# Kernel optimization log

Measured on AMD Instinct MI355X. Metric: run time of the kernel, lower is better.

## Reference

```python
import jax, jax.numpy as jnp
from jax import lax
import numpy as np

K_RAW, S_RAW, P_RAW = 4, 2, 1
K_CORR, S_CORR, P_CORR, D_CORR = 3, 1, 1, 1
FUSE_K = 3
SOFTMAX_SCALE = 10.0
NEG_BIG = -1e9  # stands in for -inf added to masked patches (softmax -> ~0)


def _patches(img, k, s, p, d=1):
    # (n,c,h,w) -> (n, c*k*k, ho, wo); channel ordering (c, kh, kw) matches torch.nn.functional.unfold
    return lax.conv_general_dilated_patches(img, (k, k), (s, s), [(p, p), (p, p)], rhs_dilation=(d, d))


def _conv_eye(m, kern):
    # 2D conv with the 'eye' fuse kernel, stride 1, same padding
    pad = (FUSE_K - 1) // 2
    return lax.conv_general_dilated(m, kern, (1, 1), [(pad, pad), (pad, pad)],
                                    dimension_numbers=('NCHW', 'OIHW', 'NCHW'))


def _deconv(score, filt, k, s, p):
    # torch conv_transpose2d for one sample: score (L,h,w), filt (L,c,k,k) -> (c, H, W)
    rhs = jnp.flip(filt.transpose(1, 0, 2, 3), (2, 3))  # (c, L, k, k), spatially flipped
    pad = k - 1 - p
    out = lax.conv_general_dilated(score[None], rhs, (1, 1), [(pad, pad), (pad, pad)],
                                   lhs_dilation=(s, s),
                                   dimension_numbers=('NCHW', 'OIHW', 'NCHW'))
    return out[0]


def _forward(x, context, mask):
    n, c, h, w = x.shape
    # --- raw context patches (patch-copy filters), torch unfold order ---
    raw_p = _patches(context, K_RAW, S_RAW, P_RAW)           # (n, c*16, hr, wr)
    hr, wr = raw_p.shape[2], raw_p.shape[3]
    Lr = hr * wr
    raw_filter = raw_p.reshape(n, c * K_RAW * K_RAW, Lr).transpose(0, 2, 1)
    raw_filter = raw_filter.reshape(n, Lr, c, K_RAW, K_RAW)
    xs = x[:, :, ::2, ::2]
    cs = context[:, :, ::2, ::2]
    # --- L2-normalized context patches for correlation ---
    cp = _patches(cs, K_CORR, S_CORR, P_CORR, D_CORR)        # (n, c*9, hu, wu)
    hu, wu = cp.shape[2], cp.shape[3]
    L = hu * wu
    cols = cp.reshape(n, c * K_CORR * K_CORR, L).transpose(0, 2, 1)  # (n, L, c*9)
    norm = jnp.sqrt(jnp.sum(cols * cols, axis=2, keepdims=True))
    cols = cols / jnp.maximum(norm, jnp.asarray(1e-4, cols.dtype))
    # --- patch correlation: grouped conv == einsum over unfolded x ---
    xp = _patches(xs, K_CORR, S_CORR, P_CORR, D_CORR)        # (n, c*9, hm, wm)
    hm, wm = xp.shape[2], xp.shape[3]
    corr = jnp.einsum('nkhw,nlk->nlhw', xp, cols)            # (n, L, hm, wm)
    # --- fuse correlation map with eye kernels (literal translation) ---
    eye = jnp.eye(FUSE_K, dtype=corr.dtype).reshape(1, 1, FUSE_K, FUSE_K)
    m_ = corr.transpose(0, 2, 3, 1).reshape(n, 1, hm * wm, hu * wu)
    m_ = _conv_eye(m_, eye)
    m_ = m_.reshape(n, hu, wu, hm, wm).transpose(0, 2, 1, 4, 3).reshape(n, 1, hu * wu, hm * wm)
    m_ = _conv_eye(m_, eye)
    corr = m_.reshape(n, wu, hu, wm, hm).transpose(0, 4, 3, 2, 1).reshape(n, -1, hu, wu)
    # --- mask: any masked pixel in a patch => patch excluded from softmax ---
    ms = mask[:, :, ::2, ::2]
    mp = _patches(ms, K_CORR, S_CORR, P_CORR, D_CORR)        # (n, 9, hu, wu)
    masked = (jnp.sum(mp, axis=1) > 0).reshape(n, L, 1, 1)
    corr = corr + jnp.where(masked, jnp.asarray(NEG_BIG, corr.dtype), jnp.asarray(0.0, corr.dtype))
    # --- softmax over patch dim ---
    att = jax.nn.softmax(corr * SOFTMAX_SCALE, axis=1)       # (n, L, hu, wu)
    # --- weighted patch copy via per-sample conv_transpose ---
    out = jax.vmap(lambda a, f: _deconv(a, f, K_RAW, S_RAW, P_RAW))(att, raw_filter)  # (n, c, h, w)
    # --- overlap normalization ---
    ones_in = jnp.ones((1, hu, wu), att.dtype)
    ones_f = jnp.ones((1, 1, K_RAW, K_RAW), att.dtype)
    overlap = _deconv(ones_in, ones_f, K_RAW, S_RAW, P_RAW)  # (1, h, w)
    overlap = jnp.where(overlap == 0, jnp.asarray(1.0, att.dtype), overlap)
    out = out / overlap[None]
    att_score = att.reshape(n, hu, wu, hu, wu)
    return out, att_score


def setup_inputs() -> dict:
    key = jax.random.key(0)
    k1, k2 = jax.random.split(key)
    N, C, H, W = 4, 96, 96, 96
    x = jax.random.normal(k1, (N, C, H, W), jnp.float32)
    context = jax.random.normal(k2, (N, C, H, W), jnp.float32)
    # rectangular inpainting hole (1 = masked), as in DeepFill training
    mask = jnp.zeros((N, 1, H, W), jnp.float32).at[:, :, 32:64, 32:64].set(1.0)
    return {"x": x, "context": context, "mask": mask}


def reference(x, context, mask):
    return _forward(x, context, mask)
```

## Files before the change

kernel.cpp:

```cpp
#include <hip/hip_runtime.h>
#include <stdint.h>

#define BN_ 4
#define CC 96
#define HF 96
#define WF 96
#define HS 48
#define WS 48
#define LL 2304
#define J2 1536
#define NEG10 (-1.0e10f)
#define NLS 32

typedef __attribute__((ext_vector_type(8))) _Float16 half8v;
typedef __attribute__((ext_vector_type(4))) float float4v;
typedef float float4u __attribute__((ext_vector_type(4), aligned(4)));

__device__ __forceinline__ int Tswap(int f) { return (f % 48) * 48 + f / 48; }

__device__ __forceinline__ unsigned short f2h(float f) {
    _Float16 h = (_Float16)f;
    return __builtin_bit_cast(unsigned short, h);
}
__device__ __forceinline__ float h2f(unsigned short u) {
    return (float)__builtin_bit_cast(_Float16, u);
}

typedef const __attribute__((address_space(1))) uint32_t* gas_ptr;
typedef __attribute__((address_space(3))) uint32_t* las_ptr;
__device__ __forceinline__ void gload16(const void* g, void* l) {
    __builtin_amdgcn_global_load_lds((gas_ptr)g, (las_ptr)l, 16, 0, 0);
}

__global__ void ssum_kernel(const float* __restrict__ ctx, float* __restrict__ ssum) {
    int idx = blockIdx.x * 256 + threadIdx.x;
    if (idx >= BN_ * HS * WS) return;
    int j = idx % WS, i = (idx / WS) % HS, n = idx / (WS * HS);
    float s = 0.f;
    for (int c = 0; c < CC; ++c) {
        float v = ctx[((size_t)(n * CC + c) * HF + 2 * i) * WF + 2 * j];
        s += v * v;
    }
    ssum[idx] = s;
}

__global__ void invnmask_kernel(const float* __restrict__ ssum, const float* __restrict__ mask,
                                float* __restrict__ invn, float* __restrict__ maskadd) {
    int idx = blockIdx.x * 256 + threadIdx.x;
    if (idx >= BN_ * LL) return;
    int l = idx % LL, n = idx / LL;
    int i0 = l / WS, j0 = l % WS;
    float s = 0.f, ms = 0.f;
    for (int dy = -1; dy <= 1; ++dy)
        for (int dx = -1; dx <= 1; ++dx) {
            int i = i0 + dy, j = j0 + dx;
            if (i >= 0 && i < HS && j >= 0 && j < WS) {
                s += ssum[(n * HS + i) * WS + j];
                ms += mask[(size_t)n * HF * WF + (2 * i) * WF + 2 * j];
            }
        }
    invn[idx] = 1.f / fmaxf(sqrtf(s), 1e-4f);
    maskadd[idx] = (ms > 0.f) ? NEG10 : 0.f;
}

__global__ void slice_split2(const float* __restrict__ ctx, const float* __restrict__ x,
                             unsigned short* __restrict__ cs_hi, unsigned short* __restrict__ cs_lo,
                             unsigned short* __restrict__ xs_hi, unsigned short* __restrict__ xs_lo) {
    int idx = blockIdx.x * 256 + threadIdx.x;
    if (idx >= BN_ * LL * CC) return;
    const float* src = blockIdx.y ? x : ctx;
    unsigned short* hi = blockIdx.y ? xs_hi : cs_hi;
    unsigned short* lo = blockIdx.y ? xs_lo : cs_lo;
    int c = idx % CC;
    int u = (idx / CC) % LL;
    int n = idx / (CC * LL);
    int i = u / WS, j = u % WS;
    float v = src[((size_t)(n * CC + c) * HF + 2 * i) * WF + 2 * j];
    unsigned short h = f2h(v);
    hi[idx] = h;
    lo[idx] = f2h(v - h2f(h));
}

__global__ void rf_split(const float* __restrict__ ctx, unsigned short* __restrict__ hf) {
    int idx = blockIdx.x * 256 + threadIdx.x;
    if (idx >= BN_ * J2 * LL) return;
    int l = idx % LL;
    int j = (idx / LL) % J2;
    int n = idx / (LL * J2);
    int c = j >> 4, ky = (j >> 2) & 3, kx = j & 3;
    int y = 2 * (l / WS) + ky - 1;
    int x = 2 * (l % WS) + kx - 1;
    float v = 0.f;
    if (y >= 0 && y < HF && x >= 0 && x < WF)
        v = ctx[((size_t)(n * CC + c) * HF + y) * WF + x];
    hf[idx] = f2h(v);
}

__global__ __launch_bounds__(256, 4) void gemm_split3(
    const unsigned short* __restrict__ Ah_, const unsigned short* __restrict__ Al_,
    const unsigned short* __restrict__ Bh_, const unsigned short* __restrict__ Bl_,
    float* __restrict__ Cout, int M_, int N_, int K_, int nbx, int nby)
{
    __shared__ unsigned short lds[4][128][32];

    int wg = blockIdx.x;
    int wgid = (wg & 7) * (gridDim.x >> 3) + (wg >> 3);
    int bx = wgid % nbx;
    int t1 = wgid / nbx;
    int by = t1 % nby;
    int bz = t1 / nby;
    const int m0 = by * 128, n0 = bx * 128;
    const int t = threadIdx.x;

    const size_t sA = (size_t)M_ * K_, sB = (size_t)N_ * K_;
    const unsigned short* Ah = Ah_ + (size_t)bz * sA;
    const unsigned short* Al = Al_ + (size_t)bz * sA;
    const unsigned short* Bh = Bh_ + (size_t)bz * sB;
    const unsigned short* Bl = Bl_ + (size_t)bz * sB;

    const int rloc = t >> 2;
    const int sst = t & 3;
    const int kg = sst ^ ((rloc >> 1) & 3);
    const size_t offA0 = (size_t)(m0 + rloc) * K_ + kg * 8;
    const size_t offA1 = (size_t)(m0 + 64 + rloc) * K_ + kg * 8;
    const size_t offB0 = (size_t)(n0 + rloc) * K_ + kg * 8;
    const size_t offB1 = (size_t)(n0 + 64 + rloc) * K_ + kg * 8;
    const unsigned short* gp0 = Ah + offA0;
    const unsigned short* gp1 = Ah + offA1;
    const unsigned short* gp2 = Al + offA0;
    const unsigned short* gp3 = Al + offA1;
    const unsigned short* gp4 = Bh + offB0;
    const unsigned short* gp5 = Bh + offB1;
    const unsigned short* gp6 = Bl + offB0;
    const unsigned short* gp7 = Bl + offB1;
    unsigned short* lp0 = &lds[0][rloc][sst * 8];
    unsigned short* lp1 = &lds[0][64 + rloc][sst * 8];
    unsigned short* lp2 = &lds[1][rloc][sst * 8];
    unsigned short* lp3 = &lds[1][64 + rloc][sst * 8];
    unsigned short* lp4 = &lds[2][rloc][sst * 8];
    unsigned short* lp5 = &lds[2][64 + rloc][sst * 8];
    unsigned short* lp6 = &lds[3][rloc][sst * 8];
    unsigned short* lp7 = &lds[3][64 + rloc][sst * 8];

    const int lane = t & 63;
    const int w = t >> 6, wr = w >> 1, wc = w & 1;
    const int lr = lane & 15, lg = lane >> 4;

    float4v acc[4][4] = {};
    const int nt = K_ / 32;

    for (int kt = 0; kt < nt; ++kt) {
        __syncthreads();
        gload16(gp0, lp0); gload16(gp1, lp1);
        gload16(gp2, lp2); gload16(gp3, lp3);
        gload16(gp4, lp4); gload16(gp5, lp5);
        gload16(gp6, lp6); gload16(gp7, lp7);
        gp0 += 32; gp1 += 32; gp2 += 32; gp3 += 32;
        gp4 += 32; gp5 += 32; gp6 += 32; gp7 += 32;
        __syncthreads();

        half8v bh[4], bl[4];
#pragma unroll
        for (int j = 0; j < 4; ++j) {
            int row = wc * 64 + j * 16 + lr;
            int s = (lg ^ ((row >> 1) & 3)) * 8;
            bh[j] = *(const half8v*)&lds[2][row][s];
            bl[j] = *(const half8v*)&lds[3][row][s];
        }
#pragma unroll
        for (int i = 0; i < 4; ++i) {
            int row = wr * 64 + i * 16 + lr;
            int s = (lg ^ ((row >> 1) & 3)) * 8;
            half8v ah = *(const half8v*)&lds[0][row][s];
            half8v al = *(const half8v*)&lds[1][row][s];
#pragma unroll
            for (int j = 0; j < 4; ++j) {
                acc[i][j] = __builtin_amdgcn_mfma_f32_16x16x32_f16(ah, bh[j], acc[i][j], 0, 0, 0);
                acc[i][j] = __builtin_amdgcn_mfma_f32_16x16x32_f16(ah, bl[j], acc[i][j], 0, 0, 0);
                acc[i][j] = __builtin_amdgcn_mfma_f32_16x16x32_f16(al, bh[j], acc[i][j], 0, 0, 0);
            }
        }
    }

    float* Cb = Cout + (size_t)bz * M_ * N_;
#pragma unroll
    for (int i = 0; i < 4; ++i) {
        int mb = m0 + wr * 64 + i * 16 + lg * 4;
#pragma unroll
        for (int j = 0; j < 4; ++j) {
            int nn = n0 + wc * 64 + j * 16 + lr;
#pragma unroll
            for (int r = 0; r < 4; ++r)
                Cb[(size_t)(mb + r) * N_ + nn] = acc[i][j][r];
        }
    }
}

__global__ __launch_bounds__(256, 4) void gemm_k64(
    const unsigned short* __restrict__ Ah_, const unsigned short* __restrict__ Bh_,
    unsigned short* __restrict__ Cout, int M_, int N_, int K_, int nbx, int nby)
{
    __shared__ unsigned short lds[2][128][64];

    int wg = blockIdx.x;
    int wgid = (wg & 7) * (gridDim.x >> 3) + (wg >> 3);
    int bx = wgid % nbx;
    int t1 = wgid / nbx;
    int by = t1 % nby;
    int bz = t1 / nby;
    const int m0 = by * 128, n0 = bx * 128;
    const int t = threadIdx.x;

    const unsigned short* Ah = Ah_ + (size_t)bz * M_ * K_;
    const unsigned short* Bh = Bh_ + (size_t)bz * N_ * K_;

    const unsigned short* gpA[4];
    const unsigned short* gpB[4];
    int lo[4];
#pragma unroll
    for (int rep = 0; rep < 4; ++rep) {
        int slot = t + rep * 256;
        int row = slot >> 3, sc = slot & 7;
        int kg = sc ^ (row & 7);
        gpA[rep] = Ah + (size_t)(m0 + row) * K_ + kg * 8;
        gpB[rep] = Bh + (size_t)(n0 + row) * K_ + kg * 8;
        lo[rep] = row * 64 + sc * 8;
    }

    const int lane = t & 63;
    const int w = t >> 6, wr = w >> 1, wc = w & 1;
    const int lr = lane & 15, lg = lane >> 4;

    float4v acc[4][4] = {};
    const int nt = K_ / 64;
    unsigned short* LA = &lds[0][0][0];
    unsigned short* LB = &lds[1][0][0];

    for (int kt = 0; kt < nt; ++kt) {
        __syncthreads();
#pragma unroll
        for (int rep = 0; rep < 4; ++rep) {
            gload16(gpA[rep], LA + lo[rep]);
            gload16(gpB[rep], LB + lo[rep]);
            gpA[rep] += 64; gpB[rep] += 64;
        }
        __syncthreads();
#pragma unroll
        for (int kk = 0; kk < 2; ++kk) {
            half8v bh[4];
#pragma unroll
            for (int j = 0; j < 4; ++j) {
                int row = wc * 64 + j * 16 + lr;
                int sc = (kk * 4 + lg) ^ (row & 7);
                bh[j] = *(const half8v*)&lds[1][row][sc * 8];
            }
#pragma unroll
            for (int i = 0; i < 4; ++i) {
                int row = wr * 64 + i * 16 + lr;
                int sc = (kk * 4 + lg) ^ (row & 7);
                half8v ah = *(const half8v*)&lds[0][row][sc * 8];
#pragma unroll
                for (int j = 0; j < 4; ++j)
                    acc[i][j] = __builtin_amdgcn_mfma_f32_16x16x32_f16(ah, bh[j], acc[i][j], 0, 0, 0);
            }
        }
    }

    unsigned short* Gb = Cout + (size_t)bz * M_ * N_;
#pragma unroll
    for (int i = 0; i < 4; ++i) {
        int mb = m0 + wr * 64 + i * 16 + lg * 4;
#pragma unroll
        for (int j = 0; j < 4; ++j) {
            int nn = n0 + wc * 64 + j * 16 + lr;
#pragma unroll
            for (int r = 0; r < 4; ++r)
                Gb[(size_t)(mb + r) * N_ + nn] = f2h(acc[i][j][r]);
        }
    }
}

__global__ void gatherS(const float* __restrict__ E, const float* __restrict__ invn,
                        float* __restrict__ S) {
    int wg = blockIdx.x;
    int wgid = (wg & 7) * (gridDim.x >> 3) + (wg >> 3);
    int idx = wgid * 256 + threadIdx.x;
    int q = idx % 288;
    int l = (idx / 288) % LL;
    int n = idx / (288 * LL);
    int p0 = q * 8;
    int li = l / WS, lj = l % WS;
    int pi = p0 / WS, pj = p0 % WS;
    const float* Eb = E + (size_t)n * LL * LL;
    float4v acc0 = {0.f, 0.f, 0.f, 0.f}, acc1 = {0.f, 0.f, 0.f, 0.f};
    bool fast = (pj >= 1) && (pj + 8 <= WS - 1);
#pragma unroll
    for (int dy = -1; dy <= 1; ++dy) {
        if (li + dy < 0 || li + dy >= HS) continue;
        if (pi + dy < 0 || pi + dy >= HS) continue;
#pragma unroll
        for (int dx = -1; dx <= 1; ++dx) {
            if (lj + dx < 0 || lj + dx >= WS) continue;
            int k = dy * WS + dx;
            const float* row = &Eb[(size_t)(l + k) * LL + p0 + k];
            float4u a = *(const float4u*)row;
            float4u b = *(const float4u*)(row + 4);
            if (fast) {
                acc0 += (float4v)a;
                acc1 += (float4v)b;
            } else {
                if (pj + dx >= 0) acc0[0] += a[0];
                acc0[1] += a[1]; acc0[2] += a[2]; acc0[3] += a[3];
                acc1[0] += b[0]; acc1[1] += b[1]; acc1[2] += b[2];
                if (pj + 7 + dx < WS) acc1[3] += b[3];
            }
        }
    }
    float iv = invn[n * LL + l];
    float* dst = &S[((size_t)n * LL + l) * LL + p0];
    *(float4v*)dst = acc0 * iv;
    *(float4v*)(dst + 4) = acc1 * iv;
}

__global__ void fuse_kernel(const float* __restrict__ S, const float* __restrict__ maskadd,
                            float* __restrict__ Sf) {
    int wg = blockIdx.x;
    int wgid = (wg & 7) * (gridDim.x >> 3) + (wg >> 3);
    int idx = wgid * 256 + threadIdx.x;
    int q = idx % 288;
    int l = (idx / 288) % LL;
    int n = idx / (288 * LL);
    int p0 = q * 8;
    const float* Sb = S + (size_t)n * LL * LL;
    int Tl = Tswap(l);
    int Tp0 = Tswap(p0);
    float4v acc0 = {0.f, 0.f, 0.f, 0.f}, acc1 = {0.f, 0.f, 0.f, 0.f};
#pragma unroll
    for (int d2 = -1; d2 <= 1; ++d2) {
        int fl = Tl + d2;
        if (fl < 0 || fl >= LL) continue;
        int fp0 = Tp0 + d2;
        if (fp0 >= LL) continue;
        int l2 = Tswap(fl);
        int ee = (fp0 < 0) ? 1 : 0;
        int p2b = Tswap(fp0 + 48 * ee) - ee;
        bool fast = (fp0 >= 0) && (fp0 + 48 * 7 < LL) && (p2b - 1 >= 0) && (p2b + 8 < LL);
        if (fast) {
#pragma unroll
            for (int d1 = -1; d1 <= 1; ++d1) {
                int l3 = l2 + d1;
                if (l3 < 0 || l3 >= LL) continue;
                const float* row = &Sb[(size_t)l3 * LL + p2b + d1];
                float4u a = *(const float4u*)row;
                float4u b = *(const float4u*)(row + 4);
                acc0 += (float4v)a;
                acc1 += (float4v)b;
            }
        } else {
            bool lo0 = (fp0 >= 0);
            bool up1 = (fp0 + 48 < LL), up2 = (fp0 + 96 < LL), up3 = (fp0 + 144 < LL);
            bool up4 = (fp0 + 192 < LL), up5 = (fp0 + 240 < LL), up6 = (fp0 + 288 < LL);
            bool up7 = (fp0 + 336 < LL);
#pragma unroll
            for (int d1 = -1; d1 <= 1; ++d1) {
                int l3 = l2 + d1;
                if (l3 < 0 || l3 >= LL) continue;
                int pc = p2b + d1;
                const float* row = &Sb[(size_t)l3 * LL + pc];
                float4u a = *(const float4u*)row;
                float4u b = *(const float4u*)(row + 4);
                if (lo0 && pc >= 0 && pc < LL)  acc0[0] += a[0];
                if (up1 && pc + 1 < LL)         acc0[1] += a[1];
                if (up2 && pc + 2 < LL)         acc0[2] += a[2];
                if (up3 && pc + 3 < LL)         acc0[3] += a[3];
                if (up4 && pc + 4 < LL)         acc1[0] += b[0];
                if (up5 && pc + 5 < LL)         acc1[1] += b[1];
                if (up6 && pc + 6 < LL)         acc1[2] += b[2];
                if (up7 && pc + 7 < LL)         acc1[3] += b[3];
            }
        }
    }
    float madd = maskadd[n * LL + l];
    float* dst = &Sf[((size_t)n * LL + l) * LL + p0];
    float4v o0, o1;
#pragma unroll
    for (int i = 0; i < 4; ++i) { o0[i] = acc0[i] * 10.f + madd; o1[i] = acc1[i] * 10.f + madd; }
    *(float4v*)dst = o0;
    *(float4v*)(dst + 4) = o1;
}

__global__ __launch_bounds__(256) void colstat_kernel(const float* __restrict__ F,
                                                      float* __restrict__ pm,
                                                      float* __restrict__ ps) {
    __shared__ float msh[4][256], ssh[4][256];
    int pb = blockIdx.x, lsp = blockIdx.y, n = blockIdx.z;
    int tq = threadIdx.x & 63;
    int tl = threadIdx.x >> 6;
    int p0 = pb * 256 + tq * 4;
    const float* Fb = F + (size_t)n * LL * LL;
    const int lspan = LL / NLS;
    float mreg[4] = {-3e38f, -3e38f, -3e38f, -3e38f};
    float sreg[4] = {0.f, 0.f, 0.f, 0.f};
    int l_end = (lsp + 1) * lspan;
    for (int l = lsp * lspan + tl; l < l_end; l += 4) {
        float4v v = *(const float4v*)&Fb[(size_t)l * LL + p0];
#pragma unroll
        for (int i = 0; i < 4; ++i) {
            float mm = fmaxf(mreg[i], v[i]);
            sreg[i] = sreg[i] * __expf(mreg[i] - mm) + __expf(v[i] - mm);
            mreg[i] = mm;
        }
    }
#pragma unroll
    for (int i = 0; i < 4; ++i) { msh[tl][tq * 4 + i] = mreg[i]; ssh[tl][tq * 4 + i] = sreg[i]; }
    __syncthreads();
    if (tl == 0) {
#pragma unroll
        for (int i = 0; i < 4; ++i) {
            float m = msh[0][tq * 4 + i], s = ssh[0][tq * 4 + i];
#pragma unroll
            for (int r = 1; r < 4; ++r) {
                float m2 = msh[r][tq * 4 + i], s2 = ssh[r][tq * 4 + i];
                float mm = fmaxf(m, m2);
                s = s * __expf(m - mm) + s2 * __expf(m2 - mm);
                m = mm;
            }
            pm[((size_t)n * NLS + lsp) * LL + p0 + i] = m;
            ps[((size_t)n * NLS + lsp) * LL + p0 + i] = s;
        }
    }
}

__global__ void mergestat_kernel(const float* __restrict__ pm, const float* __restrict__ ps,
                                 float* __restrict__ mstat, float* __restrict__ sinv) {
    int idx = blockIdx.x * 256 + threadIdx.x;
    if (idx >= BN_ * LL) return;
    int n = idx / LL, p = idx % LL;
    float m = -3e38f, s = 0.f;
    for (int q = 0; q < NLS; ++q) {
        float m2 = pm[((size_t)n * NLS + q) * LL + p];
        float s2 = ps[((size_t)n * NLS + q) * LL + p];
        float mm = fmaxf(m, m2);
        s = s * __expf(m - mm) + s2 * __expf(m2 - mm);
        m = mm;
    }
    mstat[idx] = m;
    sinv[idx] = 1.f / s;
}

__global__ __launch_bounds__(256) void finish_kernel(const float* __restrict__ F,
                                                     const float* __restrict__ mstat,
                                                     const float* __restrict__ sinv,
                                                     float* __restrict__ att,
                                                     unsigned short* __restrict__ Th) {
    __shared__ float tile[64][65];
    int n = blockIdx.z;
    int l0 = blockIdx.y * 64, p0 = blockIdx.x * 64;
    const float* Fb = F + (size_t)n * LL * LL;
    float* Ab = att + (size_t)n * LL * LL;
    int tx = threadIdx.x & 15, ty = threadIdx.x >> 4;
    float4v m4 = *(const float4v*)&mstat[n * LL + p0 + tx * 4];
    float4v s4 = *(const float4v*)&sinv[n * LL + p0 + tx * 4];
#pragma unroll
    for (int q = 0; q < 4; ++q) {
        int lr = q * 16 + ty;
        float4v v = *(const float4v*)&Fb[(size_t)(l0 + lr) * LL + p0 + tx * 4];
        float4v e;
#pragma unroll
        for (int i = 0; i < 4; ++i) e[i] = __expf(v[i] - m4[i]) * s4[i];
        *(float4v*)&Ab[(size_t)(l0 + lr) * LL + p0 + tx * 4] = e;
#pragma unroll
        for (int i = 0; i < 4; ++i) tile[lr][tx * 4 + i] = e[i];
    }
    __syncthreads();
    int pr = threadIdx.x >> 2, lq = threadIdx.x & 3;
    uint32_t u[8];
#pragma unroll
    for (int i = 0; i < 8; ++i) {
        unsigned short h0 = f2h(tile[lq * 16 + 2 * i][pr]);
        unsigned short h1 = f2h(tile[lq * 16 + 2 * i + 1][pr]);
        u[i] = (uint32_t)h0 | ((uint32_t)h1 << 16);
    }
    unsigned short* dst = &Th[((size_t)n * LL + p0 + pr) * LL + l0 + lq * 16];
    ((uint32_t*)dst)[0] = u[0]; ((uint32_t*)dst)[1] = u[1];
    ((uint32_t*)dst)[2] = u[2]; ((uint32_t*)dst)[3] = u[3];
    ((uint32_t*)dst)[4] = u[4]; ((uint32_t*)dst)[5] = u[5];
    ((uint32_t*)dst)[6] = u[6]; ((uint32_t*)dst)[7] = u[7];
}

__global__ void col2im_kernel(const unsigned short* __restrict__ G, float* __restrict__ out) {
    int idx = blockIdx.x * 256 + threadIdx.x;
    if (idx >= BN_ * CC * HF * WF) return;
    int x = idx % WF;
    int y = (idx / WF) % HF;
    int c = (idx / (WF * HF)) % CC;
    int n = idx / (WF * HF * CC);
    const unsigned short* Gb = G + (size_t)n * LL * J2;
    float acc = 0.f;
#pragma unroll
    for (int ky = 0; ky < 4; ++ky) {
        int ynum = y + 1 - ky;
        if (ynum & 1) continue;
        int iy = ynum >> 1;
        if (iy < 0 || iy >= HS) continue;
#pragma unroll
        for (int kx = 0; kx < 4; ++kx) {
            int xnum = x + 1 - kx;
            if (xnum & 1) continue;
            int ix = xnum >> 1;
            if (ix < 0 || ix >= WS) continue;
            acc += h2f(Gb[(size_t)(iy * WS + ix) * J2 + c * 16 + ky * 4 + kx]);
        }
    }
    float cy = (y == 0 || y == HF - 1) ? 1.f : 2.f;
    float cx = (x == 0 || x == WF - 1) ? 1.f : 2.f;
    out[idx] = acc / (cy * cx);
}

extern "C" void kernel_launch(void* const* d_in, const int* in_sizes, int n_in,
                              void* d_out, int out_size, void* d_ws, size_t ws_size,
                              hipStream_t stream) {
    const float* x       = (const float*)d_in[0];
    const float* context = (const float*)d_in[1];
    const float* mask    = (const float*)d_in[2];

    float* out = (float*)d_out;
    float* att_region = out + (size_t)BN_ * CC * HF * WF;

    char* wsb = (char*)d_ws;
    const size_t ESL = (size_t)BN_ * LL * CC;
    const size_t ERF = (size_t)BN_ * J2 * LL;
    unsigned short* Th = (unsigned short*)wsb;
    float* pm    = (float*)(wsb + 42467328);
    float* ps    = (float*)(wsb + 43646976);
    float* mstat = (float*)(wsb + 44826624);
    float* sinv  = (float*)(wsb + 44863488);
    float* invn  = (float*)(wsb + 44900352);
    float* ssum  = (float*)(wsb + 44937216);
    unsigned short* cs_hi = (unsigned short*)(wsb + 44974080);
    unsigned short* cs_lo = cs_hi + ESL;
    unsigned short* xs_hi = cs_lo + ESL;
    unsigned short* xs_lo = xs_hi + ESL;
    float* E = (float*)(wsb + 63700992);
    float* F = (float*)(wsb + 63700992);
    unsigned short* RF = (unsigned short*)(wsb + 63700992);
    unsigned short* G  = (unsigned short*)(wsb + 92012544);
    float* maskadd = (float*)(wsb + 148635648);
    float* S = att_region;

    ssum_kernel<<<(BN_ * HS * WS + 255) / 256, 256, 0, stream>>>(context, ssum);
    invnmask_kernel<<<(BN_ * LL + 255) / 256, 256, 0, stream>>>(ssum, mask, invn, maskadd);

    slice_split2<<<dim3((int)(ESL / 256), 2), 256, 0, stream>>>(
        context, x, cs_hi, cs_lo, xs_hi, xs_lo);

    gemm_split3<<<(LL / 128) * (LL / 128) * BN_, 256, 0, stream>>>(
        cs_hi, cs_lo, xs_hi, xs_lo, E, LL, LL, CC, LL / 128, LL / 128);

    gatherS<<<(int)((size_t)BN_ * LL * 288 / 256), 256, 0, stream>>>(E, invn, S);

    fuse_kernel<<<(int)((size_t)BN_ * LL * 288 / 256), 256, 0, stream>>>(S, maskadd, F);

    colstat_kernel<<<dim3(LL / 256, NLS, BN_), 256, 0, stream>>>(F, pm, ps);
    mergestat_kernel<<<(BN_ * LL + 255) / 256, 256, 0, stream>>>(pm, ps, mstat, sinv);
    finish_kernel<<<dim3(LL / 64, LL / 64, BN_), 256, 0, stream>>>(F, mstat, sinv, att_region, Th);

    rf_split<<<(int)(ERF / 256), 256, 0, stream>>>(context, RF);

    gemm_k64<<<(J2 / 128) * (LL / 128) * BN_, 256, 0, stream>>>(
        Th, RF, G, LL, J2, LL, J2 / 128, LL / 128);

    col2im_kernel<<<(BN_ * CC * HF * WF + 255) / 256, 256, 0, stream>>>(G, out);
}
```

Baseline: 338.9 us.

## Fuse spatial fuse-conv with column softmax statistics into one kernel

Merges fuse_kernel and colstat_kernel so the per-column online max/sum-exp statistics are computed while each fused score row is produced. This removes a full re-read of the large F matrix and one kernel launch. Each block now covers 32 rows by 256 columns, with partial stats reduced across 8 row groups in shared memory, so there are more partial blocks (72) for mergestat and the workspace layout is shifted. Fewer, heavier blocks and extra exp work in the gather loop could cut latency hiding.

```diff
diff --git a/kernel.cpp b/kernel.cpp
--- a/kernel.cpp
+++ b/kernel.cpp
@@ -10,7 +10,7 @@
 #define LL 2304
 #define J2 1536
 #define NEG10 (-1.0e10f)
-#define NLS 32
+#define NLB 72
 
 typedef __attribute__((ext_vector_type(8))) _Float16 half8v;
 typedef __attribute__((ext_vector_type(4))) float float4v;
@@ -322,113 +322,122 @@
     *(float4v*)(dst + 4) = acc1 * iv;
 }
 
-__global__ void fuse_kernel(const float* __restrict__ S, const float* __restrict__ maskadd,
-                            float* __restrict__ Sf) {
+__global__ __launch_bounds__(256) void fuse_stat(const float* __restrict__ S,
+                                                 const float* __restrict__ maskadd,
+                                                 float* __restrict__ F,
+                                                 float* __restrict__ pm,
+                                                 float* __restrict__ ps) {
+    __shared__ float msh[8][256], ssh[8][256];
     int wg = blockIdx.x;
     int wgid = (wg & 7) * (gridDim.x >> 3) + (wg >> 3);
-    int idx = wgid * 256 + threadIdx.x;
-    int q = idx % 288;
-    int l = (idx / 288) % LL;
-    int n = idx / (288 * LL);
-    int p0 = q * 8;
+    int pb = wgid % 9;
+    int t1 = wgid / 9;
+    int lb = t1 % NLB;
+    int n = t1 / NLB;
+    int tq = threadIdx.x & 31, tl = threadIdx.x >> 5;
+    int p0 = pb * 256 + tq * 8;
     const float* Sb = S + (size_t)n * LL * LL;
-    int Tl = Tswap(l);
+    const float* mb = maskadd + n * LL;
+    float* Fb = F + (size_t)n * LL * LL;
+
     int Tp0 = Tswap(p0);
-    float4v acc0 = {0.f, 0.f, 0.f, 0.f}, acc1 = {0.f, 0.f, 0.f, 0.f};
-#pragma unroll
-    for (int d2 = -1; d2 <= 1; ++d2) {
-        int fl = Tl + d2;
-        if (fl < 0 || fl >= LL) continue;
-        int fp0 = Tp0 + d2;
-        if (fp0 >= LL) continue;
-        int l2 = Tswap(fl);
+    int p2bd[3]; int fp0d[3]; bool fastd[3];
+#pragma unroll
+    for (int d = 0; d < 3; ++d) {
+        int fp0 = Tp0 + d - 1;
+        fp0d[d] = fp0;
         int ee = (fp0 < 0) ? 1 : 0;
         int p2b = Tswap(fp0 + 48 * ee) - ee;
-        bool fast = (fp0 >= 0) && (fp0 + 48 * 7 < LL) && (p2b - 1 >= 0) && (p2b + 8 < LL);
-        if (fast) {
-#pragma unroll
-            for (int d1 = -1; d1 <= 1; ++d1) {
-                int l3 = l2 + d1;
-                if (l3 < 0 || l3 >= LL) continue;
-                const float* row = &Sb[(size_t)l3 * LL + p2b + d1];
-                float4u a = *(const float4u*)row;
-                float4u b = *(const float4u*)(row + 4);
-                acc0 += (float4v)a;
-                acc1 += (float4v)b;
+        p2bd[d] = p2b;
+        fastd[d] = (fp0 >= 0) && (fp0 + 48 * 7 < LL) && (p2b - 1 >= 0) && (p2b + 8 < LL);
+    }
+
+    float m0r = -3e38f, m1r = -3e38f, m2r = -3e38f, m3r = -3e38f;
+    float m4r = -3e38f, m5r = -3e38f, m6r = -3e38f, m7r = -3e38f;
+    float s0r = 0.f, s1r = 0.f, s2r = 0.f, s3r = 0.f;
+    float s4r = 0.f, s5r = 0.f, s6r = 0.f, s7r = 0.f;
+
+#define STATUP(mr, sr, fv) do { float mm_ = fmaxf(mr, fv); \
+        sr = sr * __expf(mr - mm_) + __expf(fv - mm_); mr = mm_; } while (0)
+
+    for (int it = 0; it < 4; ++it) {
+        int l = lb * 32 + it * 8 + tl;
+        int Tl = Tswap(l);
+        float4v acc0 = {0.f, 0.f, 0.f, 0.f}, acc1 = {0.f, 0.f, 0.f, 0.f};
+#pragma unroll
+        for (int d = 0; d < 3; ++d) {
+            int fl = Tl + d - 1;
+            if (fl < 0 || fl >= LL) continue;
+            int fp0 = fp0d[d];
+            if (fp0 >= LL) continue;
+            int l2 = Tswap(fl);
+            int p2b = p2bd[d];
+            if (fastd[d]) {
+#pragma unroll
+                for (int d1 = -1; d1 <= 1; ++d1) {
+                    int l3 = l2 + d1;
+                    if (l3 < 0 || l3 >= LL) continue;
+                    const float* row = &Sb[(size_t)l3 * LL + p2b + d1];
+                    float4u a = *(const float4u*)row;
+                    float4u b = *(const float4u*)(row + 4);
+                    acc0 += (float4v)a;
+                    acc1 += (float4v)b;
+                }
+            } else {
+                bool lo0 = (fp0 >= 0);
+                bool up1 = (fp0 + 48 < LL), up2 = (fp0 + 96 < LL), up3 = (fp0 + 144 < LL);
+                bool up4 = (fp0 + 192 < LL), up5 = (fp0 + 240 < LL), up6 = (fp0 + 288 < LL);
+                bool up7 = (fp0 + 336 < LL);
+#pragma unroll
+                for (int d1 = -1; d1 <= 1; ++d1) {
+                    int l3 = l2 + d1;
+                    if (l3 < 0 || l3 >= LL) continue;
+                    int pc = p2b + d1;
+                    const float* row = &Sb[(size_t)l3 * LL + pc];
+                    float4u a = *(const float4u*)row;
+                    float4u b = *(const float4u*)(row + 4);
+                    if (lo0 && pc >= 0 && pc < LL)  acc0[0] += a[0];
+                    if (up1 && pc + 1 < LL)         acc0[1] += a[1];
+                    if (up2 && pc + 2 < LL)         acc0[2] += a[2];
+                    if (up3 && pc + 3 < LL)         acc0[3] += a[3];
+                    if (up4 && pc + 4 < LL)         acc1[0] += b[0];
+                    if (up5 && pc + 5 < LL)         acc1[1] += b[1];
+                    if (up6 && pc + 6 < LL)         acc1[2] += b[2];
+                    if (up7 && pc + 7 < LL)         acc1[3] += b[3];
+                }
             }
-        } else {
-            bool lo0 = (fp0 >= 0);
-            bool up1 = (fp0 + 48 < LL), up2 = (fp0 + 96 < LL), up3 = (fp0 + 144 < LL);
-            bool up4 = (fp0 + 192 < LL), up5 = (fp0 + 240 < LL), up6 = (fp0 + 288 < LL);
-            bool up7 = (fp0 + 336 < LL);
-#pragma unroll
-            for (int d1 = -1; d1 <= 1; ++d1) {
-                int l3 = l2 + d1;
-                if (l3 < 0 || l3 >= LL) continue;
-                int pc = p2b + d1;
-                const float* row = &Sb[(size_t)l3 * LL + pc];
-                float4u a = *(const float4u*)row;
-                float4u b = *(const float4u*)(row + 4);
-                if (lo0 && pc >= 0 && pc < LL)  acc0[0] += a[0];
-                if (up1 && pc + 1 < LL)         acc0[1] += a[1];
-                if (up2 && pc + 2 < LL)         acc0[2] += a[2];
-                if (up3 && pc + 3 < LL)         acc0[3] += a[3];
-                if (up4 && pc + 4 < LL)         acc1[0] += b[0];
-                if (up5 && pc + 5 < LL)         acc1[1] += b[1];
-                if (up6 && pc + 6 < LL)         acc1[2] += b[2];
-                if (up7 && pc + 7 < LL)         acc1[3] += b[3];
-            }
-        }
-    }
-    float madd = maskadd[n * LL + l];
-    float* dst = &Sf[((size_t)n * LL + l) * LL + p0];
-    float4v o0, o1;
-#pragma unroll
-    for (int i = 0; i < 4; ++i) { o0[i] = acc0[i] * 10.f + madd; o1[i] = acc1[i] * 10.f + madd; }
-    *(float4v*)dst = o0;
-    *(float4v*)(dst + 4) = o1;
-}
-
-__global__ __launch_bounds__(256) void colstat_kernel(const float* __restrict__ F,
-                                                      float* __restrict__ pm,
-                                                      float* __restrict__ ps) {
-    __shared__ float msh[4][256], ssh[4][256];
-    int pb = blockIdx.x, lsp = blockIdx.y, n = blockIdx.z;
-    int tq = threadIdx.x & 63;
-    int tl = threadIdx.x >> 6;
-    int p0 = pb * 256 + tq * 4;
-    const float* Fb = F + (size_t)n * LL * LL;
-    const int lspan = LL / NLS;
-    float mreg[4] = {-3e38f, -3e38f, -3e38f, -3e38f};
-    float sreg[4] = {0.f, 0.f, 0.f, 0.f};
-    int l_end = (lsp + 1) * lspan;
-    for (int l = lsp * lspan + tl; l < l_end; l += 4) {
-        float4v v = *(const float4v*)&Fb[(size_t)l * LL + p0];
-#pragma unroll
-        for (int i = 0; i < 4; ++i) {
-            float mm = fmaxf(mreg[i], v[i]);
-            sreg[i] = sreg[i] * __expf(mreg[i] - mm) + __expf(v[i] - mm);
-            mreg[i] = mm;
-        }
-    }
-#pragma unroll
-    for (int i = 0; i < 4; ++i) { msh[tl][tq * 4 + i] = mreg[i]; ssh[tl][tq * 4 + i] = sreg[i]; }
+        }
+        float madd = mb[l];
+        float4v o0, o1;
+#pragma unroll
+        for (int i = 0; i < 4; ++i) { o0[i] = acc0[i] * 10.f + madd; o1[i] = acc1[i] * 10.f + madd; }
+        float* dst = &Fb[(size_t)l * LL + p0];
+        *(float4v*)dst = o0;
+        *(float4v*)(dst + 4) = o1;
+        STATUP(m0r, s0r, o0[0]); STATUP(m1r, s1r, o0[1]);
+        STATUP(m2r, s2r, o0[2]); STATUP(m3r, s3r, o0[3]);
+        STATUP(m4r, s4r, o1[0]); STATUP(m5r, s5r, o1[1]);
+        STATUP(m6r, s6r, o1[2]); STATUP(m7r, s7r, o1[3]);
+    }
+#undef STATUP
+
+    int base = tq * 8;
+    msh[tl][base + 0] = m0r; msh[tl][base + 1] = m1r; msh[tl][base + 2] = m2r; msh[tl][base + 3] = m3r;
+    msh[tl][base + 4] = m4r; msh[tl][base + 5] = m5r; msh[tl][base + 6] = m6r; msh[tl][base + 7] = m7r;
+    ssh[tl][base + 0] = s0r; ssh[tl][base + 1] = s1r; ssh[tl][base + 2] = s2r; ssh[tl][base + 3] = s3r;
+    ssh[tl][base + 4] = s4r; ssh[tl][base + 5] = s5r; ssh[tl][base + 6] = s6r; ssh[tl][base + 7] = s7r;
     __syncthreads();
-    if (tl == 0) {
-#pragma unroll
-        for (int i = 0; i < 4; ++i) {
-            float m = msh[0][tq * 4 + i], s = ssh[0][tq * 4 + i];
-#pragma unroll
-            for (int r = 1; r < 4; ++r) {
-                float m2 = msh[r][tq * 4 + i], s2 = ssh[r][tq * 4 + i];
-                float mm = fmaxf(m, m2);
-                s = s * __expf(m - mm) + s2 * __expf(m2 - mm);
-                m = mm;
-            }
-            pm[((size_t)n * NLS + lsp) * LL + p0 + i] = m;
-            ps[((size_t)n * NLS + lsp) * LL + p0 + i] = s;
-        }
-    }
+    int pcol = threadIdx.x;
+    float m = msh[0][pcol], s = ssh[0][pcol];
+#pragma unroll
+    for (int r = 1; r < 8; ++r) {
+        float m2 = msh[r][pcol], s2 = ssh[r][pcol];
+        float mm = fmaxf(m, m2);
+        s = s * __expf(m - mm) + s2 * __expf(m2 - mm);
+        m = mm;
+    }
+    pm[((size_t)n * NLB + lb) * LL + pb * 256 + pcol] = m;
+    ps[((size_t)n * NLB + lb) * LL + pb * 256 + pcol] = s;
 }
 
 __global__ void mergestat_kernel(const float* __restrict__ pm, const float* __restrict__ ps,
@@ -437,9 +446,9 @@
     if (idx >= BN_ * LL) return;
     int n = idx / LL, p = idx % LL;
     float m = -3e38f, s = 0.f;
-    for (int q = 0; q < NLS; ++q) {
-        float m2 = pm[((size_t)n * NLS + q) * LL + p];
-        float s2 = ps[((size_t)n * NLS + q) * LL + p];
+    for (int q = 0; q < NLB; ++q) {
+        float m2 = pm[((size_t)n * NLB + q) * LL + p];
+        float s2 = ps[((size_t)n * NLB + q) * LL + p];
         float mm = fmaxf(m, m2);
         s = s * __expf(m - mm) + s2 * __expf(m2 - mm);
         m = mm;
@@ -532,12 +541,12 @@
     const size_t ERF = (size_t)BN_ * J2 * LL;
     unsigned short* Th = (unsigned short*)wsb;
     float* pm    = (float*)(wsb + 42467328);
-    float* ps    = (float*)(wsb + 43646976);
-    float* mstat = (float*)(wsb + 44826624);
-    float* sinv  = (float*)(wsb + 44863488);
-    float* invn  = (float*)(wsb + 44900352);
-    float* ssum  = (float*)(wsb + 44937216);
-    unsigned short* cs_hi = (unsigned short*)(wsb + 44974080);
+    float* ps    = (float*)(wsb + 45121536);
+    float* mstat = (float*)(wsb + 47775744);
+    float* sinv  = (float*)(wsb + 47812608);
+    float* invn  = (float*)(wsb + 47849472);
+    float* ssum  = (float*)(wsb + 47886336);
+    unsigned short* cs_hi = (unsigned short*)(wsb + 47923200);
     unsigned short* cs_lo = cs_hi + ESL;
     unsigned short* xs_hi = cs_lo + ESL;
     unsigned short* xs_lo = xs_hi + ESL;
@@ -559,9 +568,7 @@
 
     gatherS<<<(int)((size_t)BN_ * LL * 288 / 256), 256, 0, stream>>>(E, invn, S);
 
-    fuse_kernel<<<(int)((size_t)BN_ * LL * 288 / 256), 256, 0, stream>>>(S, maskadd, F);
-
-    colstat_kernel<<<dim3(LL / 256, NLS, BN_), 256, 0, stream>>>(F, pm, ps);
+    fuse_stat<<<9 * NLB * BN_, 256, 0, stream>>>(S, maskadd, F, pm, ps);
     mergestat_kernel<<<(BN_ * LL + 255) / 256, 256, 0, stream>>>(pm, ps, mstat, sinv);
     finish_kernel<<<dim3(LL / 64, LL / 64, BN_), 256, 0, stream>>>(F, mstat, sinv, att_region, Th);
 
```

Result: slower. 345.8 us (+2.1%).
